# Optimization experiments

Measured on AMD Instinct MI355X. Metric: run time of the kernel, lower is better.

Reference implementation:

```python
import jax, jax.numpy as jnp
import numpy as np

S, D, H, DK, DV = 4096, 1024, 16, 64, 64


def setup_inputs() -> dict:
    key = jax.random.key(0)
    ks = jax.random.split(key, 6)
    x = jax.random.normal(ks[0], (S, D), dtype=jnp.float32)
    # per-head projection weights, stacked over heads; scaled for numerical sanity
    Wq = jax.random.normal(ks[1], (H, D, DK), dtype=jnp.float32) / np.sqrt(D)
    Wk = jax.random.normal(ks[2], (H, D, DK), dtype=jnp.float32) / np.sqrt(D)
    Wv = jax.random.normal(ks[3], (H, D, DV), dtype=jnp.float32) / np.sqrt(D)
    Wc = jax.random.normal(ks[4], (H * DV, D), dtype=jnp.float32) / np.sqrt(H * DV)
    bc = jnp.zeros((D,), dtype=jnp.float32)
    return {"x": x, "Wq": Wq, "Wk": Wk, "Wv": Wv, "Wc": Wc, "bc": bc}


def reference(x, Wq, Wk, Wv, Wc, bc):
    # Per-head projections (original loops over heads with separate Linears;
    # stacking over h is the same math, vectorized).
    q = jnp.einsum("sd,hdk->hsk", x, Wq)   # [H,S,DK]
    k = jnp.einsum("sd,hdk->hsk", x, Wk)   # [H,S,DK]
    v = jnp.einsum("sd,hdv->hsv", x, Wv)   # [H,S,DV]
    scores = jnp.einsum("hsk,htk->hst", q, k) / jnp.sqrt(jnp.asarray(DK, x.dtype))
    probs = jax.nn.softmax(scores, axis=-1)  # softmax over last dim, per row
    o = jnp.einsum("hst,htv->hsv", probs, v)  # [H,S,DV]
    cat = jnp.transpose(o, (1, 0, 2)).reshape(S, H * DV)  # concat heads on last dim
    return cat @ Wc + bc  # output projection with bias
```

## Files before the change

kernel.cpp:

```cpp
#include <hip/hip_runtime.h>
#include <hip/hip_bf16.h>

#define S_ 4096
#define D_ 1024
#define H_ 16
#define DK_ 64
#define DV_ 64

typedef short bf16x8 __attribute__((ext_vector_type(8)));
typedef short bf16x4 __attribute__((ext_vector_type(4)));
typedef float floatx4 __attribute__((ext_vector_type(4)));
using bf16 = __hip_bfloat16;

#define MFMA16(a, b, c) __builtin_amdgcn_mfma_f32_16x16x32_bf16(a, b, c, 0, 0, 0)

#if __has_builtin(__builtin_amdgcn_exp2f)
#define EXP2(x) __builtin_amdgcn_exp2f(x)
#else
#define EXP2(x) exp2f(x)
#endif

__device__ __forceinline__ void stage16(const void* g, void* l) {
    __builtin_amdgcn_global_load_lds(
        (const __attribute__((address_space(1))) void*)g,
        (__attribute__((address_space(3))) void*)l, 16, 0, 0);
}

__device__ __forceinline__ bf16x8 ldsfrag(const bf16* base, int row, int chunk) {
    return *(const bf16x8*)(base + row * 64 + (((chunk ^ (row & 7))) << 3));
}
__device__ __forceinline__ bf16x8 ldsfrag32(const bf16* base, int row, int chunk) {
    return *(const bf16x8*)(base + row * 32 + (((chunk ^ (row & 3))) << 3));
}

__device__ __forceinline__ unsigned short bfbits(float f) {
    union { bf16 h; unsigned short u; } c; c.h = __float2bfloat16(f); return c.u;
}
__device__ __forceinline__ float bf2f(bf16 h) { return __bfloat162float(h); }
__device__ __forceinline__ unsigned int pkrne(float lo, float hi) {
    return (unsigned int)bfbits(lo) | ((unsigned int)bfbits(hi) << 16);
}

__device__ __forceinline__ unsigned int pktrunc(float lo, float hi) {
    union { float f; unsigned int u; } a, b;
    a.f = hi; b.f = lo;
    return __builtin_amdgcn_perm(a.u, b.u, 0x07060302u);
}

#define WAITCNT_BAR(N)                                        \
    do {                                                      \
        asm volatile("s_waitcnt vmcnt(" #N ")" ::: "memory"); \
        __builtin_amdgcn_sched_barrier(0);                    \
        __builtin_amdgcn_s_barrier();                         \
    } while (0)

__global__ __launch_bounds__(256)
void prep(const float* __restrict__ x, const float* __restrict__ Wq,
          const float* __restrict__ Wk, const float* __restrict__ Wv,
          const float* __restrict__ Wc,
          bf16* __restrict__ xb, bf16* __restrict__ Wt, bf16* __restrict__ Wct)
{
    __shared__ float ls[64][65];
    const int bx = blockIdx.x, t = threadIdx.x;

    if (bx < 2048) {
        int i = bx * 2048 + t * 8;
        float4 a = *(const float4*)(x + i);
        float4 b = *(const float4*)(x + i + 4);
        ushort4 lo, hi;
        lo.x = bfbits(a.x); lo.y = bfbits(a.y); lo.z = bfbits(a.z); lo.w = bfbits(a.w);
        hi.x = bfbits(b.x); hi.y = bfbits(b.y); hi.z = bfbits(b.z); hi.w = bfbits(b.w);
        *(ushort4*)(xb + i) = lo;
        *(ushort4*)(xb + i + 4) = hi;
        return;
    }
    if (bx < 2816) {
        const int idx = bx - 2048;
        const int z = idx >> 4, which = z >> 4, h = z & 15;
        const float* s = (which == 0 ? Wq : which == 1 ? Wk : Wv) + (size_t)h * D_ * 64;
        bf16* d = Wt + ((size_t)which * 1024 + h * 64) * D_;
        const float scale = (which == 0) ? 0.125f * 1.44269504088896340736f : 1.0f;
        const int r0 = (idx & 15) * 64;
        {
            int r = t >> 2, cseg = (t & 3) * 16;
            const float* sp = s + (size_t)(r0 + r) * 64 + cseg;
            #pragma unroll
            for (int i = 0; i < 16; i += 4) {
                float4 v = *(const float4*)(sp + i);
                ls[r][cseg + i + 0] = v.x; ls[r][cseg + i + 1] = v.y;
                ls[r][cseg + i + 2] = v.z; ls[r][cseg + i + 3] = v.w;
            }
        }
        __syncthreads();
        {
            int c = t >> 2, rseg = (t & 3) * 16;
            bf16* dp = d + (size_t)c * D_ + r0 + rseg;
            unsigned int u[8];
            #pragma unroll
            for (int i = 0; i < 8; i++)
                u[i] = pkrne(ls[rseg + 2 * i][c] * scale, ls[rseg + 2 * i + 1][c] * scale);
            uint4 o0, o1;
            o0.x = u[0]; o0.y = u[1]; o0.z = u[2]; o0.w = u[3];
            o1.x = u[4]; o1.y = u[5]; o1.z = u[6]; o1.w = u[7];
            *(uint4*)(dp)     = o0;
            *(uint4*)(dp + 8) = o1;
        }
        return;
    }
    {
        const int idx = bx - 2816;
        const int r0 = (idx & 15) * 64, c0 = (idx >> 4) * 64;
        {
            int r = t >> 2, cseg = (t & 3) * 16;
            const float* sp = Wc + (size_t)(r0 + r) * D_ + c0 + cseg;
            #pragma unroll
            for (int i = 0; i < 16; i += 4) {
                float4 v = *(const float4*)(sp + i);
                ls[r][cseg + i + 0] = v.x; ls[r][cseg + i + 1] = v.y;
                ls[r][cseg + i + 2] = v.z; ls[r][cseg + i + 3] = v.w;
            }
        }
        __syncthreads();
        {
            int c = t >> 2, rseg = (t & 3) * 16;
            bf16* dp = Wct + (size_t)(c0 + c) * D_ + r0 + rseg;
            unsigned int u[8];
            #pragma unroll
            for (int i = 0; i < 8; i++)
                u[i] = pkrne(ls[rseg + 2 * i][c], ls[rseg + 2 * i + 1][c]);
            uint4 o0, o1;
            o0.x = u[0]; o0.y = u[1]; o0.z = u[2]; o0.w = u[3];
            o1.x = u[4]; o1.y = u[5]; o1.z = u[6]; o1.w = u[7];
            *(uint4*)(dp)     = o0;
            *(uint4*)(dp + 8) = o1;
        }
    }
}

__global__ __launch_bounds__(256)
void qkv_gemm(const bf16* __restrict__ xb, const bf16* __restrict__ Wt,
              bf16* __restrict__ Qb, bf16* __restrict__ Kb, bf16* __restrict__ Vtb)
{
    const int fid = blockIdx.x + 32 * blockIdx.y;
    const int lin = (fid & 7) * 96 + (fid >> 3);
    const int m0 = (lin & 31) * 128;
    const int n0 = (lin >> 5) * 128;
    __shared__ __align__(16) bf16 xa[3][128 * 32];
    __shared__ __align__(16) bf16 wb2[3][128 * 32];

    const int t = threadIdx.x, lane = t & 63, w = t >> 6;
    const int l15 = lane & 15, quad = lane >> 4;

    auto stage_ab = [&](int buf, int kk) {
        #pragma unroll
        for (int j = 0; j < 2; j++) {
            int row = j * 64 + (t >> 2);
            int ch  = (t & 3) ^ (row & 3);
            stage16((const char*)xb + ((size_t)(m0 + row) * D_ + kk) * 2 + ch * 16,
                    (char*)&xa[buf][0] + (j * 4 + w) * 1024);
        }
        #pragma unroll
        for (int j = 0; j < 2; j++) {
            int row = j * 64 + (t >> 2);
            int ch  = (t & 3) ^ (row & 3);
            stage16((const char*)Wt + ((size_t)(n0 + row) * D_ + kk) * 2 + ch * 16,
                    (char*)&wb2[buf][0] + (j * 4 + w) * 1024);
        }
    };

    const floatx4 fz = {0.f, 0.f, 0.f, 0.f};
    floatx4 acc[2][8];
    #pragma unroll
    for (int mt = 0; mt < 2; mt++)
        #pragma unroll
        for (int nt = 0; nt < 8; nt++) acc[mt][nt] = fz;

    const int which = n0 >> 10;

    stage_ab(0, 0);
    stage_ab(1, 32);
    WAITCNT_BAR(4);

    if (which != 2) {
        #pragma unroll 1
        for (int kt = 0; kt < 32; kt++) {
            const int cur = kt % 3;
            if (kt + 2 < 32) stage_ab((kt + 2) % 3, (kt + 2) * 32);
            bf16x8 a0 = ldsfrag32(&xa[cur][0], w * 32 + l15,      quad);
            bf16x8 a1 = ldsfrag32(&xa[cur][0], w * 32 + 16 + l15, quad);
            #pragma unroll
            for (int nt = 0; nt < 8; nt++) {
                bf16x8 b = ldsfrag32(&wb2[cur][0], nt * 16 + l15, quad);
                acc[0][nt] = MFMA16(b, a0, acc[0][nt]);
                acc[1][nt] = MFMA16(b, a1, acc[1][nt]);
            }
            if (kt + 1 < 32) {
                if (kt + 2 < 32) { WAITCNT_BAR(4); } else { WAITCNT_BAR(0); }
            }
        }
        bf16* base = (which == 0) ? Qb : Kb;
        #pragma unroll
        for (int nt = 0; nt < 8; nt++) {
            int n  = n0 + nt * 16 + quad * 4;
            int hh = (n >> 6) & 15, col = n & 63;
            #pragma unroll
            for (int mt = 0; mt < 2; mt++) {
                int s = m0 + w * 32 + mt * 16 + l15;
                uint2 o;
                o.x = pkrne(acc[mt][nt][0], acc[mt][nt][1]);
                o.y = pkrne(acc[mt][nt][2], acc[mt][nt][3]);
                *(uint2*)(base + ((size_t)hh * S_ + s) * 64 + col) = o;
            }
        }
    } else {
        #pragma unroll 1
        for (int kt = 0; kt < 32; kt++) {
            const int cur = kt % 3;
            if (kt + 2 < 32) stage_ab((kt + 2) % 3, (kt + 2) * 32);
            bf16x8 a0 = ldsfrag32(&xa[cur][0], w * 32 + l15,      quad);
            bf16x8 a1 = ldsfrag32(&xa[cur][0], w * 32 + 16 + l15, quad);
            #pragma unroll
            for (int nt = 0; nt < 8; nt++) {
                bf16x8 b = ldsfrag32(&wb2[cur][0], nt * 16 + l15, quad);
                acc[0][nt] = MFMA16(a0, b, acc[0][nt]);
                acc[1][nt] = MFMA16(a1, b, acc[1][nt]);
            }
            if (kt + 1 < 32) {
                if (kt + 2 < 32) { WAITCNT_BAR(4); } else { WAITCNT_BAR(0); }
            }
        }
        #pragma unroll
        for (int nt = 0; nt < 8; nt++) {
            int n = n0 + nt * 16 + l15;
            int hh = (n >> 6) & 15, col = n & 63;
            #pragma unroll
            for (int mt = 0; mt < 2; mt++) {
                int s = m0 + w * 32 + mt * 16 + quad * 4;
                uint2 o;
                o.x = pkrne(acc[mt][nt][0], acc[mt][nt][1]);
                o.y = pkrne(acc[mt][nt][2], acc[mt][nt][3]);
                *(uint2*)(Vtb + ((size_t)hh * 64 + col) * S_ + s) = o;
            }
        }
    }
}

template<int NKT, bool FULL>
__global__ __attribute__((amdgpu_waves_per_eu(2))) __launch_bounds__(256)
void attn(const bf16* __restrict__ Qb, const bf16* __restrict__ Kb,
          const bf16* __restrict__ Vtb, bf16* __restrict__ Cat,
          bf16* __restrict__ Opart, float* __restrict__ lpart)
{
    const int fid = blockIdx.x + 16 * (blockIdx.y + 16 * blockIdx.z);
    const int xcd = fid & 7, r = fid >> 3;
    const int hz  = (r >> 4) * 8 + xcd;
    const int m0   = (r & 15) * 256;
    const int h    = hz & 15;
    const int half = hz >> 4;
    const int keybase = half * (NKT * 64);

    __shared__ __align__(16) bf16 ka[2][64 * 64];
    __shared__ __align__(16) bf16 vt[2][64 * 64];

    const int t = threadIdx.x, lane = t & 63, w = t >> 6;
    const int l15 = lane & 15, quad = lane >> 4;

    auto stage_kv = [&](int buf, int key0) {
        const char* kg = (const char*)(Kb + ((size_t)h * S_ + key0) * 64);
        #pragma unroll
        for (int j = 0; j < 2; j++) {
            int c = (j * 4 + w) * 64 + lane;
            int row = c >> 3, ch = (c & 7) ^ (row & 7);
            stage16(kg + row * 128 + ch * 16, (char*)&ka[buf][0] + (j * 4 + w) * 1024);
        }
        const char* vg = (const char*)(Vtb + (size_t)h * 64 * S_ + key0);
        #pragma unroll
        for (int j = 0; j < 2; j++) {
            int c = (j * 4 + w) * 64 + lane;
            int row = c >> 3, ch = (c & 7) ^ (row & 7);
            stage16(vg + (size_t)row * (S_ * 2) + ch * 16, (char*)&vt[buf][0] + (j * 4 + w) * 1024);
        }
    };

    bf16x8 qf[4][2];
    #pragma unroll
    for (int nq = 0; nq < 4; nq++)
        #pragma unroll
        for (int ks = 0; ks < 2; ks++)
            qf[nq][ks] = *(const bf16x8*)(Qb +
                ((size_t)h * S_ + m0 + w * 64 + nq * 16 + l15) * 64 + ks * 32 + quad * 8);

    bf16x8 ones8;
    #pragma unroll
    for (int i = 0; i < 8; i++) ones8[i] = (short)0x3F80;

    const floatx4 fz = {0.f, 0.f, 0.f, 0.f};
    floatx4 acc[4][4];
    floatx4 rsa[4];
    #pragma unroll
    for (int nq = 0; nq < 4; nq++) {
        rsa[nq] = fz;
        #pragma unroll
        for (int nt = 0; nt < 4; nt++) acc[nq][nt] = fz;
    }

    stage_kv(0, keybase);
    __syncthreads();

    #pragma unroll 1
    for (int kt = 0; kt < NKT; kt++) {
        const int cur = kt & 1;
        if (kt + 1 < NKT) stage_kv(cur ^ 1, keybase + (kt + 1) * 64);

        union bf4u { bf16x4 v; unsigned int u[2]; };
        bf4u pf[4][4];
        #pragma unroll
        for (int mk = 0; mk < 4; mk++) {
            bf16x8 a0 = ldsfrag(&ka[cur][0], mk * 16 + l15, quad);
            bf16x8 a1 = ldsfrag(&ka[cur][0], mk * 16 + l15, 4 + quad);
            floatx4 s[4];
            #pragma unroll
            for (int nq = 0; nq < 4; nq++) s[nq] = fz;
            __builtin_amdgcn_s_setprio(1);
            #pragma unroll
            for (int nq = 0; nq < 4; nq++) s[nq] = MFMA16(a0, qf[nq][0], s[nq]);
            #pragma unroll
            for (int nq = 0; nq < 4; nq++) s[nq] = MFMA16(a1, qf[nq][1], s[nq]);
            __builtin_amdgcn_s_setprio(0);
            #pragma unroll
            for (int nq = 0; nq < 4; nq++) {
                float p0 = EXP2(s[nq][0]);
                float p1 = EXP2(s[nq][1]);
                float p2 = EXP2(s[nq][2]);
                float p3 = EXP2(s[nq][3]);
                pf[mk][nq].u[0] = pktrunc(p0, p1);
                pf[mk][nq].u[1] = pktrunc(p2, p3);
            }
        }

        #pragma unroll
        for (int p = 0; p < 2; p++) {
            union { bf16x8 v8; bf16x4 v4[2]; } b8[4];
            #pragma unroll
            for (int nq = 0; nq < 4; nq++) {
                b8[nq].v4[0] = pf[2 * p + 0][nq].v;
                b8[nq].v4[1] = pf[2 * p + 1][nq].v;
            }
            __builtin_amdgcn_s_setprio(1);
            #pragma unroll
            for (int nq = 0; nq < 4; nq++)
                rsa[nq] = MFMA16(ones8, b8[nq].v8, rsa[nq]);
            __builtin_amdgcn_s_setprio(0);
            #pragma unroll
            for (int nt = 0; nt < 4; nt++) {
                const char* vb = (const char*)&vt[cur][0]
                               + (nt * 16 + l15) * 128 + (quad & 1) * 8;
                const int r7 = l15 & 7;
                union { bf16x8 v8; bf16x4 v4[2]; } a8;
                a8.v4[0] = *(const bf16x4*)(vb + (((4 * p +     (quad >> 1)) ^ r7) << 4));
                a8.v4[1] = *(const bf16x4*)(vb + (((4 * p + 2 + (quad >> 1)) ^ r7) << 4));
                __builtin_amdgcn_s_setprio(1);
                #pragma unroll
                for (int nq = 0; nq < 4; nq++)
                    acc[nq][nt] = MFMA16(a8.v8, b8[nq].v8, acc[nq][nt]);
                __builtin_amdgcn_s_setprio(0);
            }
        }
        __syncthreads();
    }

    if (FULL) {
        #pragma unroll
        for (int nq = 0; nq < 4; nq++) {
            float inv = 1.0f / rsa[nq][0];
            int q = m0 + w * 64 + nq * 16 + l15;
            #pragma unroll
            for (int nt = 0; nt < 4; nt++) {
                uint2 o;
                o.x = pktrunc(acc[nq][nt][0] * inv, acc[nq][nt][1] * inv);
                o.y = pktrunc(acc[nq][nt][2] * inv, acc[nq][nt][3] * inv);
                *(uint2*)(Cat + (size_t)q * (H_ * DV_) + h * 64 + nt * 16 + quad * 4) = o;
            }
        }
    } else {
        const size_t plane = (size_t)(half * H_ + h) * S_;
        #pragma unroll
        for (int nq = 0; nq < 4; nq++) {
            int q = m0 + w * 64 + nq * 16 + l15;
            #pragma unroll
            for (int nt = 0; nt < 4; nt++) {
                uint2 o;
                o.x = pktrunc(acc[nq][nt][0], acc[nq][nt][1]);
                o.y = pktrunc(acc[nq][nt][2], acc[nq][nt][3]);
                *(uint2*)(Opart + (plane + q) * 64 + nt * 16 + quad * 4) = o;
            }
            if (quad == 0) lpart[plane + q] = rsa[nq][0];
        }
    }
}

template<int NS>
__global__ __launch_bounds__(256)
void combineN(const bf16* __restrict__ Opart, const float* __restrict__ lpart,
              bf16* __restrict__ Cat)
{
    const int h = blockIdx.y;
    const int off = (blockIdx.x * 256 + threadIdx.x) * 8;
    const int s = off >> 6, dv = off & 63;
    float a[8] = {0.f, 0.f, 0.f, 0.f, 0.f, 0.f, 0.f, 0.f};
    float l = 0.f;
    #pragma unroll
    for (int p = 0; p < NS; p++) {
        union { bf16x8 v; bf16 e[8]; } o;
        o.v = *(const bf16x8*)(Opart + (size_t)(p * H_ + h) * S_ * 64 + off);
        #pragma unroll
        for (int i = 0; i < 8; i++) a[i] += bf2f(o.e[i]);
        l += lpart[(size_t)(p * H_ + h) * S_ + s];
    }
    float inv = 1.0f / l;
    uint4 o;
    o.x = pktrunc(a[0] * inv, a[1] * inv);
    o.y = pktrunc(a[2] * inv, a[3] * inv);
    o.z = pktrunc(a[4] * inv, a[5] * inv);
    o.w = pktrunc(a[6] * inv, a[7] * inv);
    *(uint4*)(Cat + (size_t)s * (H_ * DV_) + h * 64 + dv) = o;
}

__global__ __launch_bounds__(256)
void out_proj(const bf16* __restrict__ Cat, const bf16* __restrict__ Wct,
              const float* __restrict__ bc, float* __restrict__ out)
{
    const int fid = blockIdx.x + 32 * blockIdx.y;
    const int lin = (fid & 7) * 64 + (fid >> 3);
    const int m0 = (lin & 31) * 128;
    const int n0 = (lin >> 5) * 64;
    __shared__ __align__(16) bf16 ca[3][128 * 64];
    __shared__ __align__(16) bf16 wb2[3][64 * 64];

    const int t = threadIdx.x, lane = t & 63, w = t >> 6;
    const int l15 = lane & 15, quad = lane >> 4;

    auto stage_ab = [&](int buf, int kk) {
        #pragma unroll
        for (int j = 0; j < 4; j++) {
            int idx = j * 256 + t;
            int r = idx >> 3, c = idx & 7;
            int ch = c ^ (r & 7);
            stage16((const char*)Cat + ((size_t)(m0 + r) * D_ + kk + ch * 8) * 2,
                    (char*)&ca[buf][0] + (j * 4 + w) * 1024);
        }
        #pragma unroll
        for (int j = 0; j < 2; j++) {
            int idx = j * 256 + t;
            int r = idx >> 3, c = idx & 7;
            int ch = c ^ (r & 7);
            stage16((const char*)Wct + ((size_t)(n0 + r) * D_ + kk + ch * 8) * 2,
                    (char*)&wb2[buf][0] + (j * 4 + w) * 1024);
        }
    };

    const floatx4 fz = {0.f, 0.f, 0.f, 0.f};
    floatx4 acc[2][4];
    #pragma unroll
    for (int mt = 0; mt < 2; mt++)
        #pragma unroll
        for (int nt = 0; nt < 4; nt++) acc[mt][nt] = fz;

    stage_ab(0, 0);
    stage_ab(1, 64);
    WAITCNT_BAR(6);

    #pragma unroll 1
    for (int kt = 0; kt < 16; kt++) {
        const int cur = kt % 3;
        if (kt + 2 < 16) stage_ab((kt + 2) % 3, (kt + 2) * 64);
        #pragma unroll
        for (int ks = 0; ks < 2; ks++) {
            bf16x8 a0 = ldsfrag(&ca[cur][0], w * 32 + l15,      ks * 4 + quad);
            bf16x8 a1 = ldsfrag(&ca[cur][0], w * 32 + 16 + l15, ks * 4 + quad);
            #pragma unroll
            for (int nt = 0; nt < 4; nt++) {
                bf16x8 b = ldsfrag(&wb2[cur][0], nt * 16 + l15, ks * 4 + quad);
                acc[0][nt] = MFMA16(a0, b, acc[0][nt]);
                acc[1][nt] = MFMA16(a1, b, acc[1][nt]);
            }
        }
        if (kt + 1 < 16) {
            if (kt + 2 < 16) { WAITCNT_BAR(6); } else { WAITCNT_BAR(0); }
        }
    }

    #pragma unroll
    for (int nt = 0; nt < 4; nt++) {
        int col = n0 + nt * 16 + l15;
        float bias = bc[col];
        #pragma unroll
        for (int mt = 0; mt < 2; mt++)
            #pragma unroll
            for (int r = 0; r < 4; r++) {
                int row = m0 + w * 32 + mt * 16 + quad * 4 + r;
                out[(size_t)row * D_ + col] = acc[mt][nt][r] + bias;
            }
    }
}

extern "C" void kernel_launch(void* const* d_in, const int* in_sizes, int n_in,
                              void* d_out, int out_size, void* d_ws, size_t ws_size,
                              hipStream_t stream)
{
    const float* x  = (const float*)d_in[0];
    const float* Wq = (const float*)d_in[1];
    const float* Wk = (const float*)d_in[2];
    const float* Wv = (const float*)d_in[3];
    const float* Wc = (const float*)d_in[4];
    const float* bc = (const float*)d_in[5];
    float* out = (float*)d_out;

    bf16* xb  = (bf16*)d_ws;
    bf16* Cat = xb;
    bf16* Wt  = xb  + (size_t)S_ * D_;
    bf16* Wct = Wt  + (size_t)3 * H_ * 64 * D_;
    bf16* Qb  = Wct + (size_t)D_ * H_ * DV_;
    bf16* Kb  = Qb  + (size_t)H_ * S_ * 64;
    bf16* Vtb = Kb  + (size_t)H_ * S_ * 64;
    bf16* Opart = Vtb + (size_t)H_ * 64 * S_;

    float* lpart4 = (float*)(Opart + (size_t)4 * H_ * S_ * 64);
    float* lpart2 = (float*)(Opart + (size_t)2 * H_ * S_ * 64);
    const size_t need4 = (size_t)((char*)(lpart4 + (size_t)4 * H_ * S_) - (char*)d_ws);
    const size_t need2 = (size_t)((char*)(lpart2 + (size_t)2 * H_ * S_) - (char*)d_ws);

    prep<<<dim3(3072), 256, 0, stream>>>(x, Wq, Wk, Wv, Wc, xb, Wt, Wct);
    qkv_gemm<<<dim3(S_ / 128, 3072 / 128), 256, 0, stream>>>(xb, Wt, Qb, Kb, Vtb);

    if (ws_size >= need4) {
        attn<16, false><<<dim3(16, 16, 4), 256, 0, stream>>>(
            Qb, Kb, Vtb, Cat, Opart, lpart4);
        combineN<4><<<dim3(S_ * 64 / 2048, H_), 256, 0, stream>>>(Opart, lpart4, Cat);
    } else if (ws_size >= need2) {
        attn<32, false><<<dim3(16, 16, 2), 256, 0, stream>>>(
            Qb, Kb, Vtb, Cat, Opart, lpart2);
        combineN<2><<<dim3(S_ * 64 / 2048, H_), 256, 0, stream>>>(Opart, lpart2, Cat);
    } else {
        attn<64, true><<<dim3(16, 16, 1), 256, 0, stream>>>(
            Qb, Kb, Vtb, Cat, Opart, lpart2);
    }

    out_proj<<<dim3(S_ / 128, D_ / 64), 256, 0, stream>>>(Cat, Wct, bc, out);
}
```

Before: 219.3 us.

## Enlarge QKV GEMM tiles to 256x256 with 512 threads and K=64 steps

Reworks the QKV projection GEMM from 128x128 tiles on 256 threads to 256x256 tiles on 512 threads, with 8 waves in a 2x4 grid and each wave computing a 128x64 sub-tile. The K step goes from 32 to 64 and staging drops from triple to double buffering with a plain barrier per iteration. The aim is more data reuse per LDS load and fewer global loads per FLOP. The cost is 128 KB of LDS, heavier register pressure, and only 192 blocks, which may underfill the GPU's compute units. The new loop also no longer waits explicitly for the async LDS loads before the barrier, so correctness depends on the barrier draining them.

Measured after the change: 223.5 us. No clear change (+1.9%).

```diff
diff --git a/kernel.cpp b/kernel.cpp
--- a/kernel.cpp
+++ b/kernel.cpp
@@ -137,75 +137,79 @@
     }
 }
 
-__global__ __launch_bounds__(256)
+__global__ __attribute__((amdgpu_waves_per_eu(2))) __launch_bounds__(512)
 void qkv_gemm(const bf16* __restrict__ xb, const bf16* __restrict__ Wt,
               bf16* __restrict__ Qb, bf16* __restrict__ Kb, bf16* __restrict__ Vtb)
 {
-    const int fid = blockIdx.x + 32 * blockIdx.y;
-    const int lin = (fid & 7) * 96 + (fid >> 3);
-    const int m0 = (lin & 31) * 128;
-    const int n0 = (lin >> 5) * 128;
-    __shared__ __align__(16) bf16 xa[3][128 * 32];
-    __shared__ __align__(16) bf16 wb2[3][128 * 32];
+    const int fid = blockIdx.x + 16 * blockIdx.y;
+    const int lin = (fid & 7) * 24 + (fid >> 3);
+    const int m0 = (lin & 15) * 256;
+    const int n0 = (lin >> 4) * 256;
+    __shared__ __align__(16) bf16 xa[2][256 * 64];
+    __shared__ __align__(16) bf16 wb2[2][256 * 64];
 
     const int t = threadIdx.x, lane = t & 63, w = t >> 6;
     const int l15 = lane & 15, quad = lane >> 4;
+    const int wr = w >> 2, wc = w & 3;
 
     auto stage_ab = [&](int buf, int kk) {
         #pragma unroll
-        for (int j = 0; j < 2; j++) {
-            int row = j * 64 + (t >> 2);
-            int ch  = (t & 3) ^ (row & 3);
-            stage16((const char*)xb + ((size_t)(m0 + row) * D_ + kk) * 2 + ch * 16,
-                    (char*)&xa[buf][0] + (j * 4 + w) * 1024);
-        }
-        #pragma unroll
-        for (int j = 0; j < 2; j++) {
-            int row = j * 64 + (t >> 2);
-            int ch  = (t & 3) ^ (row & 3);
-            stage16((const char*)Wt + ((size_t)(n0 + row) * D_ + kk) * 2 + ch * 16,
-                    (char*)&wb2[buf][0] + (j * 4 + w) * 1024);
+        for (int j = 0; j < 4; j++) {
+            int idx = j * 512 + t;
+            int r = idx >> 3, c = idx & 7;
+            int ch = c ^ (r & 7);
+            stage16((const char*)xb + ((size_t)(m0 + r) * D_ + kk + ch * 8) * 2,
+                    (char*)&xa[buf][0] + (j * 8 + w) * 1024);
+        }
+        #pragma unroll
+        for (int j = 0; j < 4; j++) {
+            int idx = j * 512 + t;
+            int r = idx >> 3, c = idx & 7;
+            int ch = c ^ (r & 7);
+            stage16((const char*)Wt + ((size_t)(n0 + r) * D_ + kk + ch * 8) * 2,
+                    (char*)&wb2[buf][0] + (j * 8 + w) * 1024);
         }
     };
 
     const floatx4 fz = {0.f, 0.f, 0.f, 0.f};
-    floatx4 acc[2][8];
-    #pragma unroll
-    for (int mt = 0; mt < 2; mt++)
-        #pragma unroll
-        for (int nt = 0; nt < 8; nt++) acc[mt][nt] = fz;
+    floatx4 acc[8][4];
+    #pragma unroll
+    for (int mt = 0; mt < 8; mt++)
+        #pragma unroll
+        for (int nt = 0; nt < 4; nt++) acc[mt][nt] = fz;
 
     const int which = n0 >> 10;
 
     stage_ab(0, 0);
-    stage_ab(1, 32);
-    WAITCNT_BAR(4);
-
     if (which != 2) {
         #pragma unroll 1
-        for (int kt = 0; kt < 32; kt++) {
-            const int cur = kt % 3;
-            if (kt + 2 < 32) stage_ab((kt + 2) % 3, (kt + 2) * 32);
-            bf16x8 a0 = ldsfrag32(&xa[cur][0], w * 32 + l15,      quad);
-            bf16x8 a1 = ldsfrag32(&xa[cur][0], w * 32 + 16 + l15, quad);
-            #pragma unroll
-            for (int nt = 0; nt < 8; nt++) {
-                bf16x8 b = ldsfrag32(&wb2[cur][0], nt * 16 + l15, quad);
-                acc[0][nt] = MFMA16(b, a0, acc[0][nt]);
-                acc[1][nt] = MFMA16(b, a1, acc[1][nt]);
-            }
-            if (kt + 1 < 32) {
-                if (kt + 2 < 32) { WAITCNT_BAR(4); } else { WAITCNT_BAR(0); }
+        for (int kt = 0; kt < 16; kt++) {
+            const int cur = kt & 1;
+            __syncthreads();
+            if (kt < 15) stage_ab(cur ^ 1, (kt + 1) * 64);
+            #pragma unroll
+            for (int ks = 0; ks < 2; ks++) {
+                bf16x8 b[4];
+                #pragma unroll
+                for (int nt = 0; nt < 4; nt++)
+                    b[nt] = ldsfrag(&wb2[cur][0], wc * 64 + nt * 16 + l15, ks * 4 + quad);
+                #pragma unroll
+                for (int mt = 0; mt < 8; mt++) {
+                    bf16x8 a = ldsfrag(&xa[cur][0], wr * 128 + mt * 16 + l15, ks * 4 + quad);
+                    #pragma unroll
+                    for (int nt = 0; nt < 4; nt++)
+                        acc[mt][nt] = MFMA16(b[nt], a, acc[mt][nt]);
+                }
             }
         }
         bf16* base = (which == 0) ? Qb : Kb;
         #pragma unroll
-        for (int nt = 0; nt < 8; nt++) {
-            int n  = n0 + nt * 16 + quad * 4;
+        for (int nt = 0; nt < 4; nt++) {
+            int n  = n0 + wc * 64 + nt * 16 + quad * 4;
             int hh = (n >> 6) & 15, col = n & 63;
             #pragma unroll
-            for (int mt = 0; mt < 2; mt++) {
-                int s = m0 + w * 32 + mt * 16 + l15;
+            for (int mt = 0; mt < 8; mt++) {
+                int s = m0 + wr * 128 + mt * 16 + l15;
                 uint2 o;
                 o.x = pkrne(acc[mt][nt][0], acc[mt][nt][1]);
                 o.y = pkrne(acc[mt][nt][2], acc[mt][nt][3]);
@@ -214,28 +218,32 @@
         }
     } else {
         #pragma unroll 1
-        for (int kt = 0; kt < 32; kt++) {
-            const int cur = kt % 3;
-            if (kt + 2 < 32) stage_ab((kt + 2) % 3, (kt + 2) * 32);
-            bf16x8 a0 = ldsfrag32(&xa[cur][0], w * 32 + l15,      quad);
-            bf16x8 a1 = ldsfrag32(&xa[cur][0], w * 32 + 16 + l15, quad);
-            #pragma unroll
-            for (int nt = 0; nt < 8; nt++) {
-                bf16x8 b = ldsfrag32(&wb2[cur][0], nt * 16 + l15, quad);
-                acc[0][nt] = MFMA16(a0, b, acc[0][nt]);
-                acc[1][nt] = MFMA16(a1, b, acc[1][nt]);
-            }
-            if (kt + 1 < 32) {
-                if (kt + 2 < 32) { WAITCNT_BAR(4); } else { WAITCNT_BAR(0); }
-            }
-        }
-        #pragma unroll
-        for (int nt = 0; nt < 8; nt++) {
-            int n = n0 + nt * 16 + l15;
+        for (int kt = 0; kt < 16; kt++) {
+            const int cur = kt & 1;
+            __syncthreads();
+            if (kt < 15) stage_ab(cur ^ 1, (kt + 1) * 64);
+            #pragma unroll
+            for (int ks = 0; ks < 2; ks++) {
+                bf16x8 b[4];
+                #pragma unroll
+                for (int nt = 0; nt < 4; nt++)
+                    b[nt] = ldsfrag(&wb2[cur][0], wc * 64 + nt * 16 + l15, ks * 4 + quad);
+                #pragma unroll
+                for (int mt = 0; mt < 8; mt++) {
+                    bf16x8 a = ldsfrag(&xa[cur][0], wr * 128 + mt * 16 + l15, ks * 4 + quad);
+                    #pragma unroll
+                    for (int nt = 0; nt < 4; nt++)
+                        acc[mt][nt] = MFMA16(a, b[nt], acc[mt][nt]);
+                }
+            }
+        }
+        #pragma unroll
+        for (int nt = 0; nt < 4; nt++) {
+            int n = n0 + wc * 64 + nt * 16 + l15;
             int hh = (n >> 6) & 15, col = n & 63;
             #pragma unroll
-            for (int mt = 0; mt < 2; mt++) {
-                int s = m0 + w * 32 + mt * 16 + quad * 4;
+            for (int mt = 0; mt < 8; mt++) {
+                int s = m0 + wr * 128 + mt * 16 + quad * 4;
                 uint2 o;
                 o.x = pkrne(acc[mt][nt][0], acc[mt][nt][1]);
                 o.y = pkrne(acc[mt][nt][2], acc[mt][nt][3]);
@@ -531,7 +539,7 @@
     const size_t need2 = (size_t)((char*)(lpart2 + (size_t)2 * H_ * S_) - (char*)d_ws);
 
     prep<<<dim3(3072), 256, 0, stream>>>(x, Wq, Wk, Wv, Wc, xb, Wt, Wct);
-    qkv_gemm<<<dim3(S_ / 128, 3072 / 128), 256, 0, stream>>>(xb, Wt, Qb, Kb, Vtb);
+    qkv_gemm<<<dim3(16, 12), 512, 0, stream>>>(xb, Wt, Qb, Kb, Vtb);
 
     if (ws_size >= need4) {
         attn<16, false><<<dim3(16, 16, 4), 256, 0, stream>>>(
```
